# Performance work log

Hardware: AMD Instinct MI355X
Metric: run time of the kernel (lower is better)

Reference implementation:

```python
import jax, jax.numpy as jnp
import numpy as np

DEPTH = 4
V = 4          # num_variables
B = 131072     # batch


def _level_counts(D, v):
    # n[d] = number of tree nodes whose depth attribute is d
    n = [0] * (D + 1)
    n[D] = 1
    for d in range(D, 1, -1):
        n[d - 1] = n[d] * (v + 1)   # v subformulas + 1 last_subformula
    n[0] = n[1]                      # each depth-1 node has exactly one depth-0 last
    return n


def setup_inputs() -> dict:
    key = jax.random.key(0)
    n = _level_counts(DEPTH, V)
    ks = jax.random.split(key, 2 * DEPTH + 2)
    inp = {"x": jax.random.uniform(ks[0], (B, V), jnp.float32, 0.5, 1.5)}
    # depth-0 constants (one per depth-0 node), like nn.Parameter(2*randn) but
    # scaled for numerical sanity of the deep product tree
    inp["lam0"] = jax.random.normal(ks[1], (n[0],), jnp.float32)
    for d in range(1, DEPTH + 1):
        inp[f"lam{d}"] = jax.random.normal(ks[2 * d], (n[d], V), jnp.float32)
        inp[f"pow{d}"] = 0.5 * jax.random.normal(ks[2 * d + 1], (n[d], V), jnp.float32)
    return inp


def reference(x, lam0, lam1, pow1, lam2, pow2, lam3, pow3, lam4, pow4):
    # Vectorized evaluation of the recursive tree, level by level.
    # Level d holds n_d independent NestedFormula nodes; each produces a (B,) vector.
    xt = x.T  # (V, B)
    batch = x.shape[0]
    # depth-0 nodes: constant lambda broadcast over batch
    f = jnp.broadcast_to(lam0[:, None], (lam0.shape[0], batch))  # (n0, B)
    lams = [lam1, lam2, lam3, lam4]
    pows = [pow1, pow2, pow3, pow4]
    for d in range(1, DEPTH + 1):
        lam, pw = lams[d - 1], pows[d - 1]           # (n_d, V)
        xp = xt[None, :, :] ** pw[:, :, None]        # (n_d, V, B): x_i ** power_i
        if d == 1:
            # subformula_result == 1; last subformula is the matching depth-0 node
            f = jnp.einsum('nv,nvb->nb', lam, xp) + f
        else:
            # children of node j at level d are nodes j*(V+1) .. j*(V+1)+V at level d-1:
            # first V are subformulas, last one is last_subformula
            fr = f.reshape(lam.shape[0], V + 1, batch)
            f = jnp.einsum('nv,nvb->nb', lam, xp * fr[:, :V, :]) + fr[:, V, :]
    return f[0][:, None]  # (B, 1)
```

## Files before the change

kernel.cpp:

```cpp
#include <hip/hip_runtime.h>


#define VV 4

typedef float v2f __attribute__((ext_vector_type(2)));
typedef int   v2i __attribute__((ext_vector_type(2)));

__device__ __forceinline__ v2f splat(float s) { return (v2f){s, s}; }

__device__ __forceinline__ v2f pexp2(v2f t) {
    const v2f MAGIC = {12582912.0f, 12582912.0f};
    v2f tm = t + MAGIC;
    v2f nf = tm - MAGIC;
    v2f f  = t - nf;
    v2f p  = splat(1.3333558e-3f);
    p = __builtin_elementwise_fma(p, f, splat(9.6181291e-3f));
    p = __builtin_elementwise_fma(p, f, splat(5.5504109e-2f));
    p = __builtin_elementwise_fma(p, f, splat(2.4022651e-1f));
    p = __builtin_elementwise_fma(p, f, splat(6.9314718e-1f));
    p = __builtin_elementwise_fma(p, f, splat(1.0f));
    v2i eb = __builtin_bit_cast(v2i, tm) << 23;
    v2i rb = __builtin_bit_cast(v2i, p) + eb;
    return __builtin_bit_cast(v2f, rb);
}

__device__ __forceinline__ v2f f1_eval2(int n1, const v2f lx[VV],
    const float* __restrict__ lam0, const float* __restrict__ lam1,
    const float* __restrict__ pow1)
{
    v2f a = splat(lam0[n1]);
#pragma unroll
    for (int v = 0; v < VV; ++v) {
        const float p = pow1[n1 * VV + v];
        const float l = lam1[n1 * VV + v];
        a = __builtin_elementwise_fma(splat(l), pexp2(splat(p) * lx[v]), a);
    }
    return a;
}

__device__ __forceinline__ v2f f2_eval2(int n2, const v2f lx[VV],
    const float* __restrict__ lam0, const float* __restrict__ lam1,
    const float* __restrict__ pow1, const float* __restrict__ lam2,
    const float* __restrict__ pow2)
{
    v2f acc = splat(0.f);
#pragma unroll
    for (int c1 = 0; c1 < VV; ++c1) {
        v2f f1 = f1_eval2(n2 * (VV + 1) + c1, lx, lam0, lam1, pow1);
        const float l = lam2[n2 * VV + c1];
        const float p = pow2[n2 * VV + c1];
        acc = __builtin_elementwise_fma(splat(l) * pexp2(splat(p) * lx[c1]),
                                        f1, acc);
    }
    return acc + f1_eval2(n2 * (VV + 1) + VV, lx, lam0, lam1, pow1);
}

__device__ __forceinline__ v2f f3_eval2(int n3, const v2f lx[VV],
    const float* __restrict__ lam0, const float* __restrict__ lam1,
    const float* __restrict__ pow1, const float* __restrict__ lam2,
    const float* __restrict__ pow2, const float* __restrict__ lam3,
    const float* __restrict__ pow3)
{
    v2f acc = splat(0.f);
#pragma unroll
    for (int c2 = 0; c2 < VV; ++c2) {
        v2f f2 = f2_eval2(n3 * (VV + 1) + c2, lx, lam0, lam1, pow1, lam2, pow2);
        const float l = lam3[n3 * VV + c2];
        const float p = pow3[n3 * VV + c2];
        acc = __builtin_elementwise_fma(splat(l) * pexp2(splat(p) * lx[c2]),
                                        f2, acc);
    }
    return acc + f2_eval2(n3 * (VV + 1) + VV, lx, lam0, lam1, pow1, lam2, pow2);
}

__global__ __launch_bounds__(320) void nested_formula_r10(
    const float4* __restrict__ x,
    const float*  __restrict__ lam0,
    const float*  __restrict__ lam1,
    const float*  __restrict__ pow1,
    const float*  __restrict__ lam2,
    const float*  __restrict__ pow2,
    const float*  __restrict__ lam3,
    const float*  __restrict__ pow3,
    const float*  __restrict__ lam4,
    const float*  __restrict__ pow4,
    float* __restrict__ out,
    int B)
{
    const int lane = threadIdx.x & 63;
    const int r    = threadIdx.x >> 6;
    const int b0   = blockIdx.x * 128 + lane;
    const int b1   = b0 + 64;

    __shared__ float red[5][128];

    const float4 xa = x[min(b0, B - 1)];
    const float4 xb = x[min(b1, B - 1)];
    v2f lx[VV] = {
        (v2f){ __builtin_amdgcn_logf(xa.x), __builtin_amdgcn_logf(xb.x) },
        (v2f){ __builtin_amdgcn_logf(xa.y), __builtin_amdgcn_logf(xb.y) },
        (v2f){ __builtin_amdgcn_logf(xa.z), __builtin_amdgcn_logf(xb.z) },
        (v2f){ __builtin_amdgcn_logf(xa.w), __builtin_amdgcn_logf(xb.w) } };

    v2f f3 = f3_eval2(r, lx, lam0, lam1, pow1, lam2, pow2, lam3, pow3);

    v2f part;
    if (r < 4) {
        const float l4 = lam4[r];
        const float p4 = pow4[r];
        const v2f lxr = (r == 0) ? lx[0] : (r == 1) ? lx[1]
                      : (r == 2) ? lx[2] : lx[3];
        part = splat(l4) * pexp2(splat(p4) * lxr) * f3;
    } else {
        part = f3;
    }

    red[r][lane]      = part.x;
    red[r][lane + 64] = part.y;
    __syncthreads();

    if (r == 0) {
        float sA = ((red[0][lane] + red[1][lane]) +
                    (red[2][lane] + red[3][lane])) + red[4][lane];
        float sB = ((red[0][lane + 64] + red[1][lane + 64]) +
                    (red[2][lane + 64] + red[3][lane + 64])) + red[4][lane + 64];
        if (b0 < B) out[b0] = sA;
        if (b1 < B) out[b1] = sB;
    }
}

extern "C" void kernel_launch(void* const* d_in, const int* in_sizes, int n_in,
                              void* d_out, int out_size, void* d_ws, size_t ws_size,
                              hipStream_t stream) {
    const float4* x    = (const float4*)d_in[0];
    const float*  lam0 = (const float*)d_in[1];
    const float*  lam1 = (const float*)d_in[2];
    const float*  pow1 = (const float*)d_in[3];
    const float*  lam2 = (const float*)d_in[4];
    const float*  pow2 = (const float*)d_in[5];
    const float*  lam3 = (const float*)d_in[6];
    const float*  pow3 = (const float*)d_in[7];
    const float*  lam4 = (const float*)d_in[8];
    const float*  pow4 = (const float*)d_in[9];
    float* out = (float*)d_out;

    int B = in_sizes[0] / 4;
    dim3 block(320, 1, 1);
    dim3 grid((B + 127) / 128, 1, 1);
    nested_formula_r10<<<grid, block, 0, stream>>>(
        x, lam0, lam1, pow1, lam2, pow2, lam3, pow3, lam4, pow4, out, B);
}
```

Measured before the change: 85.98 us.

## Stage tree parameters in LDS and split exp2 between hardware and polynomial units

At block start, all lambda/power parameters are copied into shared memory as interleaved (lam, pow) float2 pairs, and the tree recursion is restructured into explicit loops that read from LDS rather than from scalar global loads. Some exp2 evaluations now use the hardware transcendental unit (v_exp_f32) and the rest use the FMA polynomial, so the work is spread across the transcendental and VALU pipes. The outer c2 loop is no longer unrolled, which shrinks the code but adds loop overhead, plus an extra barrier and the LDS staging work in every block.

```diff
diff --git a/kernel.cpp b/kernel.cpp
--- a/kernel.cpp
+++ b/kernel.cpp
@@ -7,6 +7,10 @@
 typedef int   v2i __attribute__((ext_vector_type(2)));
 
 __device__ __forceinline__ v2f splat(float s) { return (v2f){s, s}; }
+
+__device__ __forceinline__ v2f texp2(v2f t) {
+    return (v2f){ __builtin_amdgcn_exp2f(t.x), __builtin_amdgcn_exp2f(t.y) };
+}
 
 __device__ __forceinline__ v2f pexp2(v2f t) {
     const v2f MAGIC = {12582912.0f, 12582912.0f};
@@ -19,80 +23,43 @@
     p = __builtin_elementwise_fma(p, f, splat(2.4022651e-1f));
     p = __builtin_elementwise_fma(p, f, splat(6.9314718e-1f));
     p = __builtin_elementwise_fma(p, f, splat(1.0f));
-    v2i eb = __builtin_bit_cast(v2i, tm) << 23;
-    v2i rb = __builtin_bit_cast(v2i, p) + eb;
+    v2i rb = __builtin_bit_cast(v2i, p) + (__builtin_bit_cast(v2i, tm) << 23);
     return __builtin_bit_cast(v2f, rb);
 }
 
-__device__ __forceinline__ v2f f1_eval2(int n1, const v2f lx[VV],
-    const float* __restrict__ lam0, const float* __restrict__ lam1,
-    const float* __restrict__ pow1)
+#define L0_OFF  0
+#define LP1_OFF 128
+#define LP2_OFF 1128
+#define LP3_OFF 1328
+#define LP4_OFF 1368
+#define P_TOTAL 1376
+
+__global__ __launch_bounds__(320) void nested_formula_r11(
+    const float4* __restrict__ x,
+    const float*  __restrict__ lam0, const float* __restrict__ lam1,
+    const float*  __restrict__ pow1, const float* __restrict__ lam2,
+    const float*  __restrict__ pow2, const float* __restrict__ lam3,
+    const float*  __restrict__ pow3, const float* __restrict__ lam4,
+    const float*  __restrict__ pow4,
+    float* __restrict__ out, int B)
 {
-    v2f a = splat(lam0[n1]);
-#pragma unroll
-    for (int v = 0; v < VV; ++v) {
-        const float p = pow1[n1 * VV + v];
-        const float l = lam1[n1 * VV + v];
-        a = __builtin_elementwise_fma(splat(l), pexp2(splat(p) * lx[v]), a);
-    }
-    return a;
-}
+    __shared__ float sp[P_TOTAL];
+    __shared__ float red[5][128];
 
-__device__ __forceinline__ v2f f2_eval2(int n2, const v2f lx[VV],
-    const float* __restrict__ lam0, const float* __restrict__ lam1,
-    const float* __restrict__ pow1, const float* __restrict__ lam2,
-    const float* __restrict__ pow2)
-{
-    v2f acc = splat(0.f);
-#pragma unroll
-    for (int c1 = 0; c1 < VV; ++c1) {
-        v2f f1 = f1_eval2(n2 * (VV + 1) + c1, lx, lam0, lam1, pow1);
-        const float l = lam2[n2 * VV + c1];
-        const float p = pow2[n2 * VV + c1];
-        acc = __builtin_elementwise_fma(splat(l) * pexp2(splat(p) * lx[c1]),
-                                        f1, acc);
-    }
-    return acc + f1_eval2(n2 * (VV + 1) + VV, lx, lam0, lam1, pow1);
-}
-
-__device__ __forceinline__ v2f f3_eval2(int n3, const v2f lx[VV],
-    const float* __restrict__ lam0, const float* __restrict__ lam1,
-    const float* __restrict__ pow1, const float* __restrict__ lam2,
-    const float* __restrict__ pow2, const float* __restrict__ lam3,
-    const float* __restrict__ pow3)
-{
-    v2f acc = splat(0.f);
-#pragma unroll
-    for (int c2 = 0; c2 < VV; ++c2) {
-        v2f f2 = f2_eval2(n3 * (VV + 1) + c2, lx, lam0, lam1, pow1, lam2, pow2);
-        const float l = lam3[n3 * VV + c2];
-        const float p = pow3[n3 * VV + c2];
-        acc = __builtin_elementwise_fma(splat(l) * pexp2(splat(p) * lx[c2]),
-                                        f2, acc);
-    }
-    return acc + f2_eval2(n3 * (VV + 1) + VV, lx, lam0, lam1, pow1, lam2, pow2);
-}
-
-__global__ __launch_bounds__(320) void nested_formula_r10(
-    const float4* __restrict__ x,
-    const float*  __restrict__ lam0,
-    const float*  __restrict__ lam1,
-    const float*  __restrict__ pow1,
-    const float*  __restrict__ lam2,
-    const float*  __restrict__ pow2,
-    const float*  __restrict__ lam3,
-    const float*  __restrict__ pow3,
-    const float*  __restrict__ lam4,
-    const float*  __restrict__ pow4,
-    float* __restrict__ out,
-    int B)
-{
-    const int lane = threadIdx.x & 63;
-    const int r    = threadIdx.x >> 6;
+    const int tid  = threadIdx.x;
+    const int lane = tid & 63;
+    const int r    = tid >> 6;
     const int b0   = blockIdx.x * 128 + lane;
     const int b1   = b0 + 64;
 
-    __shared__ float red[5][128];
+    for (int i = tid; i < 125; i += 320) sp[L0_OFF + i] = lam0[i];
+    for (int i = tid; i < 500; i += 320) {
+        sp[LP1_OFF + 2 * i]     = lam1[i];
+        sp[LP1_OFF + 2 * i + 1] = pow1[i];
+    }
+    if (tid < 100) { sp[LP2_OFF + 2*tid] = lam2[tid]; sp[LP2_OFF + 2*tid+1] = pow2[tid]; }
+    if (tid < 20)  { sp[LP3_OFF + 2*tid] = lam3[tid]; sp[LP3_OFF + 2*tid+1] = pow3[tid]; }
+    if (tid < 4)   { sp[LP4_OFF + 2*tid] = lam4[tid]; sp[LP4_OFF + 2*tid+1] = pow4[tid]; }
 
     const float4 xa = x[min(b0, B - 1)];
     const float4 xb = x[min(b1, B - 1)];
@@ -102,15 +69,55 @@
         (v2f){ __builtin_amdgcn_logf(xa.z), __builtin_amdgcn_logf(xb.z) },
         (v2f){ __builtin_amdgcn_logf(xa.w), __builtin_amdgcn_logf(xb.w) } };
 
-    v2f f3 = f3_eval2(r, lx, lam0, lam1, pow1, lam2, pow2, lam3, pow3);
+    __syncthreads();
+
+    const float2* lp1 = (const float2*)(sp + LP1_OFF);
+    const float2* lp2 = (const float2*)(sp + LP2_OFF);
+    const float2* lp3 = (const float2*)(sp + LP3_OFF);
+
+    v2f acc3 = splat(0.f), last3 = splat(0.f);
+    for (int c2 = 0; c2 < 5; ++c2) {
+        const int n2 = r * 5 + c2;
+        v2f acc2 = splat(0.f), last2 = splat(0.f);
+#pragma unroll
+        for (int c1 = 0; c1 < 5; ++c1) {
+            const int n1 = n2 * 5 + c1;
+            const float2 a0 = lp1[n1 * 4 + 0];
+            const float2 a1 = lp1[n1 * 4 + 1];
+            const float2 a2 = lp1[n1 * 4 + 2];
+            const float2 a3 = lp1[n1 * 4 + 3];
+            v2f f1 = splat(sp[L0_OFF + n1]);
+            f1 = __builtin_elementwise_fma(splat(a0.x), texp2(splat(a0.y) * lx[0]), f1);
+            f1 = __builtin_elementwise_fma(splat(a1.x), texp2(splat(a1.y) * lx[1]), f1);
+            f1 = __builtin_elementwise_fma(splat(a2.x), pexp2(splat(a2.y) * lx[2]), f1);
+            f1 = __builtin_elementwise_fma(splat(a3.x), pexp2(splat(a3.y) * lx[3]), f1);
+            if (c1 < 4) {
+                const float2 lp = lp2[n2 * 4 + c1];
+                acc2 = __builtin_elementwise_fma(
+                    splat(lp.x) * texp2(splat(lp.y) * lx[c1]), f1, acc2);
+            } else {
+                last2 = f1;
+            }
+        }
+        v2f f2 = acc2 + last2;
+        if (c2 < 4) {
+            const float2 lp = lp3[r * 4 + c2];
+            const v2f lxc = (c2 == 0) ? lx[0] : (c2 == 1) ? lx[1]
+                          : (c2 == 2) ? lx[2] : lx[3];
+            acc3 = __builtin_elementwise_fma(
+                splat(lp.x) * texp2(splat(lp.y) * lxc), f2, acc3);
+        } else {
+            last3 = f2;
+        }
+    }
+    v2f f3 = acc3 + last3;
 
     v2f part;
     if (r < 4) {
-        const float l4 = lam4[r];
-        const float p4 = pow4[r];
+        const float2 lp = *(const float2*)(sp + LP4_OFF + 2 * r);
         const v2f lxr = (r == 0) ? lx[0] : (r == 1) ? lx[1]
                       : (r == 2) ? lx[2] : lx[3];
-        part = splat(l4) * pexp2(splat(p4) * lxr) * f3;
+        part = splat(lp.x) * texp2(splat(lp.y) * lxr) * f3;
     } else {
         part = f3;
     }
@@ -147,6 +154,6 @@
     int B = in_sizes[0] / 4;
     dim3 block(320, 1, 1);
     dim3 grid((B + 127) / 128, 1, 1);
-    nested_formula_r10<<<grid, block, 0, stream>>>(
+    nested_formula_r11<<<grid, block, 0, stream>>>(
         x, lam0, lam1, pow1, lam2, pow2, lam3, pow3, lam4, pow4, out, B);
 }
```

Result: no change. 84.91 us (-1.2%).
